# Optimization experiments

Hardware: AMD Instinct MI355X
Metric: run time of the kernel (lower is better)

## Reference

```python
import jax, jax.numpy as jnp
import numpy as np

DROPOUT_P = 0.5


def normalize_adj(A):
    # A_tilda = A + I ; A_hat = D^-0.5 A_tilda D^-0.5
    # The torch code does this with diag_embed + two bmm (O(N^3));
    # mathematically it is row/col broadcasting (O(N^2)).
    B, N, _ = A.shape
    A_tilda = A + jnp.eye(N, dtype=A.dtype)
    d_inv_sqrt = jnp.sum(A_tilda, axis=2) ** -0.5          # [B, N]
    return d_inv_sqrt[:, :, None] * A_tilda * d_inv_sqrt[:, None, :]


def gcn_layer(X, A_hat, W, b):
    # standard Kipf GCN layer: A_hat @ (X @ W) + b
    return jnp.einsum('bnm,bmd->bnd', A_hat, X @ W) + b


def setup_inputs() -> dict:
    key = jax.random.key(0)
    ks = jax.random.split(key, 6)
    B, N, Din, H, C = 8, 2048, 64, 64, 16
    X = jax.random.normal(ks[0], (B, N, Din), dtype=jnp.float32)
    A = jax.random.uniform(ks[1], (B, N, N), dtype=jnp.float32)
    W1 = jax.random.normal(ks[2], (Din, H), dtype=jnp.float32) * (1.0 / np.sqrt(Din))
    b1 = jax.random.normal(ks[3], (H,), dtype=jnp.float32) * 0.01
    W2 = jax.random.normal(ks[4], (H, C), dtype=jnp.float32) * (1.0 / np.sqrt(H))
    b2 = jax.random.normal(ks[5], (C,), dtype=jnp.float32) * 0.01
    return {"X": X, "A": A, "W1": W1, "b1": b1, "W2": W2, "b2": b2}


def reference(X, A, W1, b1, W2, b2):
    A_hat = normalize_adj(A)
    h = jax.nn.relu(gcn_layer(X, A_hat, W1, b1))
    # F.dropout default training=True -> apply dropout with a fixed key
    keep = jax.random.bernoulli(jax.random.key(42), 1.0 - DROPOUT_P, h.shape)
    h = jnp.where(keep, h / (1.0 - DROPOUT_P), 0.0).astype(h.dtype)
    return gcn_layer(h, A_hat, W2, b2)
```

## Files before the change

kernel.cpp:

```cpp
#include <hip/hip_runtime.h>

#define BN 16384
#define NN 2048
#define DD 64
#define CC 16

typedef short bf16x8 __attribute__((ext_vector_type(8)));
typedef float f32x4 __attribute__((ext_vector_type(4)));
typedef unsigned short u16x4 __attribute__((ext_vector_type(4)));

__device__ __forceinline__ f32x4 mfma16(bf16x8 a, bf16x8 b, f32x4 c) {
  return __builtin_amdgcn_mfma_f32_16x16x32_bf16(a, b, c, 0, 0, 0);
}
__device__ __forceinline__ unsigned short f2bf(float f) {
  unsigned u = __float_as_uint(f);
  return (unsigned short)((u + 0x7FFFu + ((u >> 16) & 1u)) >> 16);
}
__device__ __forceinline__ float bf2f(unsigned short h) {
  return __uint_as_float(((unsigned)h) << 16);
}
__device__ __forceinline__ bf16x8 pack8(float4 lo, float4 hi) {
  bf16x8 r;
  r[0] = (short)f2bf(lo.x); r[1] = (short)f2bf(lo.y);
  r[2] = (short)f2bf(lo.z); r[3] = (short)f2bf(lo.w);
  r[4] = (short)f2bf(hi.x); r[5] = (short)f2bf(hi.y);
  r[6] = (short)f2bf(hi.z); r[7] = (short)f2bf(hi.w);
  return r;
}

__device__ __forceinline__ unsigned tf_bits(unsigned i) {
  unsigned x0 = 0u;
  unsigned x1 = i;
  const unsigned k0 = 0u, k1 = 42u, k2 = 0x1BD11BDAu ^ 0u ^ 42u;
  x0 += k0; x1 += k1;
#define TFR(r) { x0 += x1; x1 = (x1 << (r)) | (x1 >> (32 - (r))); x1 ^= x0; }
  TFR(13) TFR(15) TFR(26) TFR(6)
  x0 += k1; x1 += k2 + 1u;
  TFR(17) TFR(29) TFR(16) TFR(24)
  x0 += k2; x1 += k0 + 2u;
  TFR(13) TFR(15) TFR(26) TFR(6)
  x0 += k0; x1 += k1 + 3u;
  TFR(17) TFR(29) TFR(16) TFR(24)
  x0 += k1; x1 += k2 + 4u;
  TFR(13) TFR(15) TFR(26) TFR(6)
  x0 += k2; x1 += k0 + 5u;
#undef TFR
  return x0 ^ x1;
}


__global__ __launch_bounds__(256) void k_pre(const float* __restrict__ A,
    const float* __restrict__ X, const float* __restrict__ W1,
    float* __restrict__ dis, unsigned short* __restrict__ Y1s)
{
  const int w = threadIdx.x >> 6, lane = threadIdx.x & 63;
  const size_t row = (size_t)blockIdx.x * 4 + w;
  const float4* Arow = (const float4*)(A + row * NN);
  float s = 0.f;
#pragma unroll
  for (int it = 0; it < 8; ++it) {
    float4 v = Arow[lane + 64 * it];
    s += (v.x + v.y) + (v.z + v.w);
  }
#pragma unroll
  for (int m = 32; m; m >>= 1) s += __shfl_xor(s, m, 64);
  const float dv = 1.0f / sqrtf(s + 1.0f);
  if (lane == 0) dis[row] = dv;
  const float* Xr = X + row * DD;
  float acc = 0.f;
#pragma unroll
  for (int k = 0; k < DD; ++k) acc += Xr[k] * W1[k * DD + lane];
  Y1s[row * DD + lane] = f2bf(dv * acc);
}

__global__ __launch_bounds__(256) void k_tr(const unsigned short* __restrict__ Y1s,
    unsigned short* __restrict__ Y1sT)
{
  __shared__ unsigned short lds[64][80];
  const int tid = threadIdx.x;
  const int r0 = blockIdx.x * 64;
  const int b = r0 >> 11, kr0 = r0 & (NN - 1);
  {
    const int rl = tid >> 2, c0 = (tid & 3) * 16;
    const u16x4* src = (const u16x4*)(Y1s + ((size_t)r0 + rl) * DD + c0);
    u16x4 v0 = src[0], v1 = src[1], v2 = src[2], v3 = src[3];
    *(u16x4*)&lds[rl][c0 + 0]  = v0;
    *(u16x4*)&lds[rl][c0 + 4]  = v1;
    *(u16x4*)&lds[rl][c0 + 8]  = v2;
    *(u16x4*)&lds[rl][c0 + 12] = v3;
  }
  __syncthreads();
  {
    const int dim = tid >> 2, rs = (tid & 3) * 16;
    u16x4 o0, o1, o2, o3;
#pragma unroll
    for (int j = 0; j < 4; ++j) {
      o0[j] = lds[rs + j][dim];
      o1[j] = lds[rs + 4 + j][dim];
      o2[j] = lds[rs + 8 + j][dim];
      o3[j] = lds[rs + 12 + j][dim];
    }
    u16x4* dst = (u16x4*)(Y1sT + ((size_t)b * DD + dim) * NN + kr0 + rs);
    dst[0] = o0; dst[1] = o1; dst[2] = o2; dst[3] = o3;
  }
}

__global__ __launch_bounds__(256, 4) void k_gemm1f(const float* __restrict__ A,
    const unsigned short* __restrict__ Y1sT, const unsigned short* __restrict__ Y1s,
    const float* __restrict__ dis, const float* __restrict__ b1,
    const float* __restrict__ W2,
    unsigned short* __restrict__ Y2sT, float* __restrict__ S2d)
{
  __shared__ float red[4][16][68];
  __shared__ float W2l[DD * CC];
  const int tid = threadIdx.x;
  *(float4*)(W2l + tid * 4) = *(const float4*)(W2 + tid * 4);
  const int Mb = blockIdx.x;
  const int w = __builtin_amdgcn_readfirstlane((int)tid >> 6);
  const int lane = tid & 63;
  const int m15 = lane & 15, quad = lane >> 4;
  const int b = Mb >> 7;
  const int k0 = w * 512 + quad * 8;
  const float* Apf = A + ((size_t)Mb * 16 + m15) * NN + k0;
  const unsigned short* Bp0 = Y1sT + ((size_t)b * DD + m15) * NN + k0;
  const unsigned short* Bp1 = Bp0 + (size_t)16 * NN;
  const unsigned short* Bp2 = Bp0 + (size_t)32 * NN;
  const unsigned short* Bp3 = Bp0 + (size_t)48 * NN;
  const f32x4 zero = 0.f;
  f32x4 acc[4];
  acc[0] = zero; acc[1] = zero; acc[2] = zero; acc[3] = zero;
  float4 fa0 = *(const float4*)Apf, fa1 = *(const float4*)(Apf + 4);
  bf16x8 b0 = *(const bf16x8*)Bp0, b1v = *(const bf16x8*)Bp1;
  bf16x8 b2v = *(const bf16x8*)Bp2, b3v = *(const bf16x8*)Bp3;
#pragma unroll 1
  for (int kk = 0; kk < 16; ++kk) {
    const int off = (kk < 15) ? (kk + 1) * 32 : 0;
    float4 na0 = *(const float4*)(Apf + off);
    float4 na1 = *(const float4*)(Apf + off + 4);
    bf16x8 nb0 = *(const bf16x8*)(Bp0 + off);
    bf16x8 nb1 = *(const bf16x8*)(Bp1 + off);
    bf16x8 nb2 = *(const bf16x8*)(Bp2 + off);
    bf16x8 nb3 = *(const bf16x8*)(Bp3 + off);
    const bf16x8 a = pack8(fa0, fa1);
    acc[0] = mfma16(a, b0,  acc[0]);
    acc[1] = mfma16(a, b1v, acc[1]);
    acc[2] = mfma16(a, b2v, acc[2]);
    acc[3] = mfma16(a, b3v, acc[3]);
    fa0 = na0; fa1 = na1; b0 = nb0; b1v = nb1; b2v = nb2; b3v = nb3;
  }
#pragma unroll
  for (int ni = 0; ni < 4; ++ni)
#pragma unroll
    for (int r = 0; r < 4; ++r)
      red[w][quad * 4 + r][ni * 16 + m15] = acc[ni][r];
  __syncthreads();
  const int rowl = tid >> 4, c0 = (tid & 15) * 4;
  f32x4 sum = *(const f32x4*)&red[0][rowl][c0];
  sum += *(const f32x4*)&red[1][rowl][c0];
  sum += *(const f32x4*)&red[2][rowl][c0];
  sum += *(const f32x4*)&red[3][rowl][c0];
  const int grow = Mb * 16 + rowl;
  const u16x4 y1d = *(const u16x4*)(Y1s + (size_t)grow * DD + c0);
  const float4 b1q = *(const float4*)(b1 + c0);
  const float dv = dis[grow];
  const unsigned o0i = (unsigned)grow * DD + c0;
  f32x4 hq;
#pragma unroll
  for (int j = 0; j < 4; ++j) {
    const float z = sum[j] + bf2f(y1d[j]);
    const float bj = j == 0 ? b1q.x : j == 1 ? b1q.y : j == 2 ? b1q.z : b1q.w;
    float h = fmaxf(dv * z + bj, 0.f);
    const unsigned bits = tf_bits(o0i + j);
    hq[j] = (bits >> 31) ? 0.f : (h + h);
  }
  __syncthreads();
  *(f32x4*)&red[0][rowl][c0] = hq;
  __syncthreads();
  const float* hrow = &red[0][rowl][0];
  const int c2 = tid & 15;
  float s = 0.f;
#pragma unroll
  for (int k = 0; k < DD; ++k) s += hrow[k] * W2l[k * CC + c2];
  const float y2 = dv * s;
  S2d[(size_t)grow * CC + c2] = y2;
  const int kr = grow & (NN - 1);
  Y2sT[((size_t)b * CC + c2) * NN + kr] = f2bf(y2);
}

__global__ __launch_bounds__(256, 4) void k_gemm2o(const float* __restrict__ A,
    const unsigned short* __restrict__ Y2sT, const float* __restrict__ S2d,
    const float* __restrict__ dis, const float* __restrict__ b2,
    float* __restrict__ out)
{
  __shared__ float red[4][16][20];
  const int Mb = blockIdx.x;
  const int w = __builtin_amdgcn_readfirstlane((int)threadIdx.x >> 6);
  const int lane = threadIdx.x & 63;
  const int m15 = lane & 15, quad = lane >> 4;
  const int b = Mb >> 7;
  const int k0 = w * 512 + quad * 8;
  const float* Apf = A + ((size_t)Mb * 16 + m15) * NN + k0;
  const unsigned short* Bp = Y2sT + ((size_t)b * CC + m15) * NN + k0;
  f32x4 acc = 0.f;
  float4 fa0 = *(const float4*)Apf, fa1 = *(const float4*)(Apf + 4);
  bf16x8 bb = *(const bf16x8*)Bp;
#pragma unroll 1
  for (int kk = 0; kk < 16; ++kk) {
    const int off = (kk < 15) ? (kk + 1) * 32 : 0;
    float4 na0 = *(const float4*)(Apf + off);
    float4 na1 = *(const float4*)(Apf + off + 4);
    bf16x8 nbb = *(const bf16x8*)(Bp + off);
    const bf16x8 a = pack8(fa0, fa1);
    acc = mfma16(a, bb, acc);
    fa0 = na0; fa1 = na1; bb = nbb;
  }
#pragma unroll
  for (int r = 0; r < 4; ++r)
    red[w][quad * 4 + r][m15] = acc[r];
  __syncthreads();
  const int tid = threadIdx.x;
  const int rowl = tid >> 4, c = tid & 15;
  const float sum = red[0][rowl][c] + red[1][rowl][c]
                  + red[2][rowl][c] + red[3][rowl][c];
  const int grow = Mb * 16 + rowl;
  out[(size_t)grow * CC + c] =
      dis[grow] * (sum + S2d[(size_t)grow * CC + c]) + b2[c];
}

#define FKS1 4
#define FKS2 16

__global__ __launch_bounds__(256) void d_deg_xw(const float* __restrict__ A,
    const float* __restrict__ X, const float* __restrict__ W1,
    float* __restrict__ dis, float* __restrict__ Y1s)
{
  const int w = threadIdx.x >> 6, lane = threadIdx.x & 63;
  const int row = __builtin_amdgcn_readfirstlane(blockIdx.x * 4 + w);
  const float4* Arow = (const float4*)(A + (size_t)row * NN);
  float s = 0.f;
#pragma unroll
  for (int it = 0; it < 8; ++it) {
    float4 v = Arow[lane + 64 * it];
    s += v.x + v.y + v.z + v.w;
  }
#pragma unroll
  for (int m = 32; m; m >>= 1) s += __shfl_xor(s, m, 64);
  const float dv = 1.0f / sqrtf(s + 1.0f);
  if (lane == 0) dis[row] = dv;
  const float* Xr = X + (size_t)row * DD;
  float acc = 0.f;
#pragma unroll
  for (int k = 0; k < DD; ++k) acc += Xr[k] * W1[k * DD + lane];
  Y1s[(size_t)row * DD + lane] = dv * acc;
}

__global__ __launch_bounds__(256) void d_gemm1(const float* __restrict__ A,
    const float* __restrict__ Y1s, float* __restrict__ Z1)
{
  const int rb = blockIdx.x >> 2, ks = blockIdx.x & (FKS1 - 1);
  const int lane = threadIdx.x & 63;
  const int c0 = __builtin_amdgcn_readfirstlane((threadIdx.x >> 6) << 4);
  const int row = rb * 64 + lane;
  const int batch = rb >> 5;
  const int KSEG = NN / FKS1;
  const float* Arow = A + (size_t)row * NN + ks * KSEG;
  const float* Yb = Y1s + (size_t)batch * NN * DD + c0;
  const int kbase = ks * KSEG;
  float acc[16];
#pragma unroll
  for (int c = 0; c < 16; ++c) acc[c] = 0.f;
  float4 a0 = *(const float4*)(Arow);
  float4 a1 = *(const float4*)(Arow + 4);
  float4 a2 = *(const float4*)(Arow + 8);
  float4 a3 = *(const float4*)(Arow + 12);
  for (int k = 0; k < KSEG; k += 16) {
    const int kn = (k + 16 < KSEG) ? (k + 16) : 0;
    float4 n0 = *(const float4*)(Arow + kn);
    float4 n1 = *(const float4*)(Arow + kn + 4);
    float4 n2 = *(const float4*)(Arow + kn + 8);
    float4 n3 = *(const float4*)(Arow + kn + 12);
    const float* y0 = Yb + (size_t)(kbase + k) * DD;
    const float av[16] = {a0.x, a0.y, a0.z, a0.w, a1.x, a1.y, a1.z, a1.w,
                          a2.x, a2.y, a2.z, a2.w, a3.x, a3.y, a3.z, a3.w};
#pragma unroll
    for (int j = 0; j < 16; ++j) {
      const float* yr = y0 + j * DD;
#pragma unroll
      for (int c = 0; c < 16; ++c) acc[c] += av[j] * yr[c];
    }
    a0 = n0; a1 = n1; a2 = n2; a3 = n3;
  }
  float* Zp = Z1 + ((size_t)ks * BN + row) * DD + c0;
#pragma unroll
  for (int c = 0; c < 16; c += 4) {
    float4 v; v.x = acc[c]; v.y = acc[c+1]; v.z = acc[c+2]; v.w = acc[c+3];
    *(float4*)(Zp + c) = v;
  }
}

__global__ __launch_bounds__(256) void d_epi1(const float* __restrict__ Z1,
    const float* __restrict__ Y1s, const float* __restrict__ dis,
    const float* __restrict__ b1, const float* __restrict__ W2,
    float* __restrict__ Y2s)
{
  __shared__ float W2l[DD * CC];
  __shared__ float hl[4][DD];
  const int tid = threadIdx.x;
  *(float4*)(W2l + tid * 4) = *(const float4*)(W2 + tid * 4);
  const int w = tid >> 6, lane = tid & 63;
  const int row = blockIdx.x * 4 + w;
  const size_t o = (size_t)row * DD + lane;
  float z = Y1s[o];
#pragma unroll
  for (int p = 0; p < FKS1; ++p) z += Z1[(size_t)p * BN * DD + o];
  const float dv = dis[row];
  float h = fmaxf(dv * z + b1[lane], 0.f);
  const unsigned bits = tf_bits((unsigned)o);
  h = (bits >> 31) ? 0.f : (h + h);
  hl[w][lane] = h;
  __syncthreads();
  const int wr = tid >> 6, l = tid & 63;
  const int c = l & 15, kq = l >> 4;
  float p = 0.f;
#pragma unroll
  for (int kk = 0; kk < 16; ++kk)
    p += hl[wr][kq * 16 + kk] * W2l[(kq * 16 + kk) * CC + c];
  p += __shfl_xor(p, 16, 64);
  p += __shfl_xor(p, 32, 64);
  if (l < 16) {
    const int rg = blockIdx.x * 4 + wr;
    Y2s[(size_t)rg * CC + c] = dis[rg] * p;
  }
}

__global__ __launch_bounds__(256) void d_gemm2(const float* __restrict__ A,
    const float* __restrict__ Y2s, float* __restrict__ Z2)
{
  const int rb = blockIdx.x >> 4, ks = blockIdx.x & (FKS2 - 1);
  const int row = rb * 256 + threadIdx.x;
  const int batch = rb >> 3;
  const int KSEG = NN / FKS2;
  const float* Arow = A + (size_t)row * NN + ks * KSEG;
  const float* Yb = Y2s + (size_t)batch * NN * CC;
  const int kbase = ks * KSEG;
  float acc[16];
#pragma unroll
  for (int c = 0; c < 16; ++c) acc[c] = 0.f;
  float4 a0 = *(const float4*)(Arow);
  float4 a1 = *(const float4*)(Arow + 4);
  for (int k = 0; k < KSEG; k += 8) {
    const int kn = (k + 8 < KSEG) ? (k + 8) : 0;
    float4 n0 = *(const float4*)(Arow + kn);
    float4 n1 = *(const float4*)(Arow + kn + 4);
    const float av[8] = {a0.x, a0.y, a0.z, a0.w, a1.x, a1.y, a1.z, a1.w};
#pragma unroll
    for (int j = 0; j < 8; ++j) {
      const float* yr = Yb + (size_t)(kbase + k + j) * CC;
#pragma unroll
      for (int c = 0; c < 16; ++c) acc[c] += av[j] * yr[c];
    }
    a0 = n0; a1 = n1;
  }
  float* Zp = Z2 + ((size_t)ks * BN + row) * CC;
#pragma unroll
  for (int c = 0; c < 16; c += 4) {
    float4 v; v.x = acc[c]; v.y = acc[c+1]; v.z = acc[c+2]; v.w = acc[c+3];
    *(float4*)(Zp + c) = v;
  }
}

__global__ __launch_bounds__(256) void d_final(const float* __restrict__ Z2,
    const float* __restrict__ Y2s, const float* __restrict__ dis,
    const float* __restrict__ b2, float* __restrict__ out)
{
  const int gid = blockIdx.x * 256 + threadIdx.x;
  const int r = gid >> 2, q = gid & 3;
  const size_t o = (size_t)r * CC + q * 4;
  float4 s = *(const float4*)(Y2s + o);
#pragma unroll
  for (int p = 0; p < FKS2; ++p) {
    const float4 zp = *(const float4*)(Z2 + (size_t)p * BN * CC + o);
    s.x += zp.x; s.y += zp.y; s.z += zp.z; s.w += zp.w;
  }
  const float dv = dis[r];
  const float4 bb = *(const float4*)(b2 + q * 4);
  float4 res;
  res.x = dv * s.x + bb.x;
  res.y = dv * s.y + bb.y;
  res.z = dv * s.z + bb.z;
  res.w = dv * s.w + bb.w;
  *(float4*)(out + o) = res;
}

extern "C" void kernel_launch(void* const* d_in, const int* in_sizes, int n_in,
                              void* d_out, int out_size, void* d_ws, size_t ws_size,
                              hipStream_t stream) {
  const float* X  = (const float*)d_in[0];
  const float* A  = (const float*)d_in[1];
  const float* W1 = (const float*)d_in[2];
  const float* b1 = (const float*)d_in[3];
  const float* W2 = (const float*)d_in[4];
  const float* b2 = (const float*)d_in[5];
  float* out = (float*)d_out;
  char* wsb = (char*)d_ws;

  const size_t NEED = 5832704;
  if (ws_size >= NEED) {
    unsigned short* Y1s  = (unsigned short*)wsb;
    unsigned short* Y1sT = (unsigned short*)(wsb + 2097152);
    unsigned short* Y2sT = (unsigned short*)(wsb + 4194304);
    float*          S2d  = (float*)(wsb + 4718592);
    float*          dis  = (float*)(wsb + 5767168);

    k_pre   <<<BN / 4,  256, 0, stream>>>(A, X, W1, dis, Y1s);
    k_tr    <<<BN / 64, 256, 0, stream>>>(Y1s, Y1sT);
    k_gemm1f<<<BN / 16, 256, 0, stream>>>(A, Y1sT, Y1s, dis, b1, W2, Y2sT, S2d);
    k_gemm2o<<<1024,    256, 0, stream>>>(A, Y2sT, S2d, dis, b2, out);
  } else {
    float* ws  = (float*)d_ws;
    float* dis = ws;
    float* Y1s = ws + 16384;
    float* Z1  = Y1s + (size_t)BN * DD;
    float* Z2  = Z1;
    float* Y2s = Z1 + (size_t)FKS1 * BN * DD;

    d_deg_xw<<<BN / 4,     256, 0, stream>>>(A, X, W1, dis, Y1s);
    d_gemm1 <<<256 * FKS1, 256, 0, stream>>>(A, Y1s, Z1);
    d_epi1  <<<BN / 4,     256, 0, stream>>>(Z1, Y1s, dis, b1, W2, Y2s);
    d_gemm2 <<<64 * FKS2,  256, 0, stream>>>(A, Y2s, Z2);
    d_final <<<256,        256, 0, stream>>>(Z2, Y2s, dis, b2, out);
  }
}
```

Measured before the change: 277.7 us.

## Split degree pass and fuse X@W1 with transpose through LDS

The degree reduction is now its own kernel, k_deg2. The X@W1 projection moves into a new kernel that stages X tiles and W1 in shared memory, then writes both the row-major and transposed bf16 Y1 from LDS. This removes the separate transpose kernel's global reread of Y1s and the uncoalesced per-thread scalar reads of X and W1 in the old pre kernel. The launch count stays the same, but the matmul now runs with only 256 blocks, each doing 16 serial rows per wave, which may limit parallelism.

```diff
diff --git a/kernel.cpp b/kernel.cpp
--- a/kernel.cpp
+++ b/kernel.cpp
@@ -49,9 +49,8 @@
 }
 
 
-__global__ __launch_bounds__(256) void k_pre(const float* __restrict__ A,
-    const float* __restrict__ X, const float* __restrict__ W1,
-    float* __restrict__ dis, unsigned short* __restrict__ Y1s)
+__global__ __launch_bounds__(256) void k_deg2(const float* __restrict__ A,
+    float* __restrict__ dis)
 {
   const int w = threadIdx.x >> 6, lane = threadIdx.x & 63;
   const size_t row = (size_t)blockIdx.x * 4 + w;
@@ -64,45 +63,55 @@
   }
 #pragma unroll
   for (int m = 32; m; m >>= 1) s += __shfl_xor(s, m, 64);
-  const float dv = 1.0f / sqrtf(s + 1.0f);
-  if (lane == 0) dis[row] = dv;
-  const float* Xr = X + row * DD;
-  float acc = 0.f;
-#pragma unroll
-  for (int k = 0; k < DD; ++k) acc += Xr[k] * W1[k * DD + lane];
-  Y1s[row * DD + lane] = f2bf(dv * acc);
-}
-
-__global__ __launch_bounds__(256) void k_tr(const unsigned short* __restrict__ Y1s,
-    unsigned short* __restrict__ Y1sT)
-{
-  __shared__ unsigned short lds[64][80];
+  if (lane == 0) dis[row] = 1.0f / sqrtf(s + 1.0f);
+}
+
+__global__ __launch_bounds__(256) void k_y1(const float* __restrict__ X,
+    const float* __restrict__ W1, const float* __restrict__ dis,
+    unsigned short* __restrict__ Y1s, unsigned short* __restrict__ Y1sT)
+{
+  __shared__ float Xl[64 * DD];
+  __shared__ float W1l[DD * DD];
+  __shared__ unsigned short y1t[64][80];
   const int tid = threadIdx.x;
   const int r0 = blockIdx.x * 64;
+  {
+    const float4* xs = (const float4*)(X + (size_t)r0 * DD);
+    float4* xd = (float4*)Xl;
+    const float4* ws = (const float4*)W1;
+    float4* wd = (float4*)W1l;
+#pragma unroll
+    for (int i = 0; i < 4; ++i) {
+      xd[tid + 256 * i] = xs[tid + 256 * i];
+      wd[tid + 256 * i] = ws[tid + 256 * i];
+    }
+  }
+  __syncthreads();
+  const int w = tid >> 6, lane = tid & 63;
+#pragma unroll 1
+  for (int rr = 0; rr < 16; ++rr) {
+    const int r = w * 16 + rr;
+    const float dv = dis[r0 + r];
+    float acc = 0.f;
+#pragma unroll
+    for (int k = 0; k < DD; ++k) acc += Xl[r * DD + k] * W1l[k * DD + lane];
+    const unsigned short v = f2bf(dv * acc);
+    y1t[r][lane] = v;
+    Y1s[((size_t)r0 + r) * DD + lane] = v;
+  }
+  __syncthreads();
   const int b = r0 >> 11, kr0 = r0 & (NN - 1);
-  {
-    const int rl = tid >> 2, c0 = (tid & 3) * 16;
-    const u16x4* src = (const u16x4*)(Y1s + ((size_t)r0 + rl) * DD + c0);
-    u16x4 v0 = src[0], v1 = src[1], v2 = src[2], v3 = src[3];
-    *(u16x4*)&lds[rl][c0 + 0]  = v0;
-    *(u16x4*)&lds[rl][c0 + 4]  = v1;
-    *(u16x4*)&lds[rl][c0 + 8]  = v2;
-    *(u16x4*)&lds[rl][c0 + 12] = v3;
-  }
-  __syncthreads();
-  {
-    const int dim = tid >> 2, rs = (tid & 3) * 16;
-    u16x4 o0, o1, o2, o3;
-#pragma unroll
-    for (int j = 0; j < 4; ++j) {
-      o0[j] = lds[rs + j][dim];
-      o1[j] = lds[rs + 4 + j][dim];
-      o2[j] = lds[rs + 8 + j][dim];
-      o3[j] = lds[rs + 12 + j][dim];
-    }
-    u16x4* dst = (u16x4*)(Y1sT + ((size_t)b * DD + dim) * NN + kr0 + rs);
-    dst[0] = o0; dst[1] = o1; dst[2] = o2; dst[3] = o3;
-  }
+  const int dim = tid >> 2, rs = (tid & 3) * 16;
+  u16x4 o0, o1, o2, o3;
+#pragma unroll
+  for (int j = 0; j < 4; ++j) {
+    o0[j] = y1t[rs + j][dim];
+    o1[j] = y1t[rs + 4 + j][dim];
+    o2[j] = y1t[rs + 8 + j][dim];
+    o3[j] = y1t[rs + 12 + j][dim];
+  }
+  u16x4* dst = (u16x4*)(Y1sT + ((size_t)b * DD + dim) * NN + kr0 + rs);
+  dst[0] = o0; dst[1] = o1; dst[2] = o2; dst[3] = o3;
 }
 
 __global__ __launch_bounds__(256, 4) void k_gemm1f(const float* __restrict__ A,
@@ -412,8 +421,8 @@
     float*          S2d  = (float*)(wsb + 4718592);
     float*          dis  = (float*)(wsb + 5767168);
 
-    k_pre   <<<BN / 4,  256, 0, stream>>>(A, X, W1, dis, Y1s);
-    k_tr    <<<BN / 64, 256, 0, stream>>>(Y1s, Y1sT);
+    k_deg2  <<<BN / 4,  256, 0, stream>>>(A, dis);
+    k_y1    <<<BN / 64, 256, 0, stream>>>(X, W1, dis, Y1s, Y1sT);
     k_gemm1f<<<BN / 16, 256, 0, stream>>>(A, Y1sT, Y1s, dis, b1, W2, Y2sT, S2d);
     k_gemm2o<<<1024,    256, 0, stream>>>(A, Y2sT, S2d, dis, b2, out);
   } else {
```

Measured after the change: 281.2 us. Within noise of the previous version (+1.3%).
